# Kernel optimization log

Measured on AMD Instinct MI355X. Metric: run time of the kernel, lower is better.

The kernel has to match this reference:

```python
import jax, jax.numpy as jnp
import numpy as np
from jax.scipy.special import logsumexp

P = 2.0          # geomloss p=2 -> cost = 0.5*|x-y|^2, eps = blur**2
BLUR = 0.05
SCALING = 0.5    # geomloss default annealing factor
K = 16           # fixed-length eps schedule (covers diameter/blur up to ~2^15)


def _softmin(eps, C, h):
    # softmin_i = -eps * logsumexp_j( h_j - C[i,j]/eps )
    return -eps * logsumexp(h[None, :] - C / eps, axis=1)


def _sinkhorn_one(x, y):
    # x, y: (N,) 1D point clouds, uniform weights a=b=1/N
    N = x.shape[0]
    C = 0.5 * (x[:, None] - y[None, :]) ** 2          # (N, N) cost, p=2
    a_log = jnp.full((N,), -jnp.log(jnp.float32(N)))
    b_log = a_log

    # geomloss scaling_parameters: diameter of the joint support (D=1)
    diam = jnp.maximum(x.max(), y.max()) - jnp.minimum(x.min(), y.min())
    eps0 = diam ** 2
    ks = jnp.arange(K)
    # schedule: [d^p, d^p, d^p*s^p, d^p*s^2p, ...] floored at blur^p
    eps_arr = jnp.maximum(BLUR ** 2, eps0 * (SCALING ** 2) ** jnp.maximum(ks - 1, 0))

    # geomloss runs the annealing loop with autograd disabled (implicit diff):
    Cs = jax.lax.stop_gradient(C)
    f = _softmin(eps_arr[0], Cs, b_log)       # potential on x
    g = _softmin(eps_arr[0], Cs.T, a_log)     # potential on y

    def body(carry, eps):
        f, g = carry
        ft = _softmin(eps, Cs, b_log + g / eps)
        gt = _softmin(eps, Cs.T, a_log + f / eps)
        return (0.5 * (f + ft), 0.5 * (g + gt)), None

    (f, g), _ = jax.lax.scan(body, (f, g), eps_arr)
    f = jax.lax.stop_gradient(f)
    g = jax.lax.stop_gradient(g)

    # last extrapolation step at eps = blur^p, with gradients (debias=False)
    eps = BLUR ** 2
    f_fin = _softmin(eps, C, b_log + g / eps)
    g_fin = _softmin(eps, C.T, a_log + f / eps)

    # OT_eps = <a, f> + <b, g>
    return jnp.mean(f_fin) + jnp.mean(g_fin)


def setup_inputs() -> dict:
    key = jax.random.key(0)
    kx, ky = jax.random.split(key)
    B, N = 16, 1536
    x = jax.random.normal(kx, (B, N), dtype=jnp.float32)
    y = jax.random.normal(ky, (B, N), dtype=jnp.float32)
    return {"x": x, "y": y}


def reference(x, y):
    # sum of per-sample Sinkhorn losses (equivalent to the Python loop)
    return jnp.sum(jax.vmap(_sinkhorn_one)(x, y))
```

## Files before the change

### kernel.cpp

```cpp
#include <hip/hip_runtime.h>
#include <math.h>


static constexpr int   BN    = 16;
static constexpr int   NP    = 1536;
static constexpr float BLUR2 = 0.0025f;
static constexpr float L2E   = 1.4426950408889634f;
static constexpr float LN2   = 0.6931471805599453f;
static constexpr float HLOG  = -7.33693691f;

#if defined(__has_builtin)
#if __has_builtin(__builtin_amdgcn_exp2f)
#define EXP2F(x) __builtin_amdgcn_exp2f(x)
#else
#define EXP2F(x) exp2f(x)
#endif
#else
#define EXP2F(x) exp2f(x)
#endif

__global__ __launch_bounds__(256) void sk_setup(const float* __restrict__ x,
                                                const float* __restrict__ y,
                                                float* __restrict__ eps0) {
    const int b = blockIdx.x;
    const int t = threadIdx.x;
    float mn = INFINITY, mx = -INFINITY;
    for (int j = t; j < NP; j += 256) {
        float xv = x[b * NP + j], yv = y[b * NP + j];
        mn = fminf(mn, fminf(xv, yv));
        mx = fmaxf(mx, fmaxf(xv, yv));
    }
    for (int o = 1; o < 64; o <<= 1) {
        mn = fminf(mn, __shfl_xor(mn, o));
        mx = fmaxf(mx, __shfl_xor(mx, o));
    }
    __shared__ float smn[4], smx[4];
    const int w = t >> 6;
    if ((t & 63) == 0) { smn[w] = mn; smx[w] = mx; }
    __syncthreads();
    if (t == 0) {
        mn = fminf(fminf(smn[0], smn[1]), fminf(smn[2], smn[3]));
        mx = fmaxf(fmaxf(smx[0], smx[1]), fmaxf(smx[2], smx[3]));
        float d = mx - mn;
        eps0[b] = d * d;
    }
}

__global__ __launch_bounds__(256) void sk_round(const float* __restrict__ x,
                                                const float* __restrict__ y,
                                                float* __restrict__ ws,
                                                float* __restrict__ out,
                                                int round) {
    __shared__ __align__(16) float2 cu[NP];
    __shared__ float wsum[4];

    const int blk    = blockIdx.x;
    const int batch  = blk / 48;
    const int rb     = blk % 48;
    const int dir    = (rb < 24) ? 0 : 1;
    const int rowblk = rb - dir * 24;

    float* F0 = ws + 16;
    float* F1 = F0 + BN * NP;
    float* G0 = F1 + BN * NP;
    float* G1 = G0 + BN * NP;
    const int ri = (round + 1) & 1;
    const int wi = round & 1;
    float* Fr = ri ? F1 : F0;  float* Fw = wi ? F1 : F0;
    float* Gr = ri ? G1 : G0;  float* Gw = wi ? G1 : G0;

    const float* colc; const float* rowc; const float* hsrc;
    float* obuf; const float* oldb;
    if (dir == 0) {
        colc = y + batch * NP; rowc = x + batch * NP;
        hsrc = Gr + batch * NP; obuf = Fw + batch * NP; oldb = Fr + batch * NP;
    } else {
        colc = x + batch * NP; rowc = y + batch * NP;
        hsrc = Fr + batch * NP; obuf = Gw + batch * NP; oldb = Gr + batch * NP;
    }

    const float e0 = ws[batch];
    float eps;
    if (round == 0)       eps = fmaxf(BLUR2, e0);
    else if (round >= 17) eps = BLUR2;
    else {
        int mk = round - 2; if (mk < 0) mk = 0;
        eps = fmaxf(BLUR2, e0 / (float)(1u << (2 * mk)));
    }
    const float ieps = 1.0f / eps;
    const float c    = 0.5f * ieps;
    const float cL   = c * L2E;

    const int t = threadIdx.x;
    for (int j = t; j < NP; j += 256) {
        float cj = colc[j];
        float hj = (round == 0) ? HLOG : fmaf(hsrc[j], ieps, HLOG);
        float U  = L2E * hj - cL * cj * cj;
        cu[j] = make_float2(cj, U);
    }
    __syncthreads();

    const int lc = t & 3;
    const int lr = t >> 2;
    const int i  = rowblk * 64 + lr;
    const float xi = rowc[i];
    const float S  = 2.0f * cL * xi;
    const float Kc = -cL * xi * xi;

    const float4* p = (const float4*)cu;

    float m0 = -INFINITY, m1 = -INFINITY;
    #pragma unroll 4
    for (int q = lc; q < NP / 2; q += 4) {
        float4 a = p[q];
        m0 = fmaxf(m0, fmaf(S, a.x, a.y));
        m1 = fmaxf(m1, fmaf(S, a.z, a.w));
    }
    float m = fmaxf(m0, m1);
    m = fmaxf(m, __shfl_xor(m, 1));
    m = fmaxf(m, __shfl_xor(m, 2));

    float s0 = 0.0f, s1 = 0.0f;
    #pragma unroll 4
    for (int q = lc; q < NP / 2; q += 4) {
        float4 a = p[q];
        s0 += EXP2F(fmaf(S, a.x, a.y) - m);
        s1 += EXP2F(fmaf(S, a.z, a.w) - m);
    }
    float s = s0 + s1;
    s += __shfl_xor(s, 1);
    s += __shfl_xor(s, 2);

    const float ft = -eps * LN2 * (m + __log2f(s) + Kc);

    if (round < 17) {
        if (lc == 0) {
            float v = (round == 0) ? ft : 0.5f * (oldb[i] + ft);
            obuf[i] = v;
        }
    } else {
        float v = (lc == 0) ? ft : 0.0f;
        for (int o = 1; o < 64; o <<= 1) v += __shfl_xor(v, o);
        const int w = t >> 6;
        if ((t & 63) == 0) wsum[w] = v;
        __syncthreads();
        if (t == 0) {
            float tot = (wsum[0] + wsum[1]) + (wsum[2] + wsum[3]);
            atomicAdd(out, tot * (1.0f / NP));
        }
    }
}

extern "C" void kernel_launch(void* const* d_in, const int* in_sizes, int n_in,
                              void* d_out, int out_size, void* d_ws, size_t ws_size,
                              hipStream_t stream) {
    const float* x = (const float*)d_in[0];
    const float* y = (const float*)d_in[1];
    float* out = (float*)d_out;
    float* ws  = (float*)d_ws;

    hipMemsetAsync(out, 0, sizeof(float), stream);
    hipLaunchKernelGGL(sk_setup, dim3(BN), dim3(256), 0, stream, x, y, ws);
    for (int r = 0; r < 18; ++r) {
        hipLaunchKernelGGL(sk_round, dim3(768), dim3(256), 0, stream,
                           x, y, ws, out, r);
    }
}
```

Before: 400.8 us.

## Register-block eight rows per 32-lane group to reuse LDS column loads

Measured after the change: 370.3 us. 1.08x faster.

```diff
diff --git a/kernel.cpp b/kernel.cpp
--- a/kernel.cpp
+++ b/kernel.cpp
@@ -95,51 +95,80 @@
     for (int j = t; j < NP; j += 256) {
         float cj = colc[j];
         float hj = (round == 0) ? HLOG : fmaf(hsrc[j], ieps, HLOG);
-        float U  = L2E * hj - cL * cj * cj;
+        float U  = fmaf(L2E, hj, -cL * cj * cj);
         cu[j] = make_float2(cj, U);
     }
     __syncthreads();
 
-    const int lc = t & 3;
-    const int lr = t >> 2;
-    const int i  = rowblk * 64 + lr;
-    const float xi = rowc[i];
-    const float S  = 2.0f * cL * xi;
-    const float Kc = -cL * xi * xi;
+    const int l  = t & 31;
+    const int g  = t >> 5;
+    const int i0 = rowblk * 64 + g * 8;
+
+    float S[8], Kc[8];
+    #pragma unroll
+    for (int r = 0; r < 8; ++r) {
+        float xi = rowc[i0 + r];
+        S[r]  = 2.0f * cL * xi;
+        Kc[r] = -cL * xi * xi;
+    }
 
     const float4* p = (const float4*)cu;
 
-    float m0 = -INFINITY, m1 = -INFINITY;
-    #pragma unroll 4
-    for (int q = lc; q < NP / 2; q += 4) {
+    float m[8];
+    #pragma unroll
+    for (int r = 0; r < 8; ++r) m[r] = -INFINITY;
+    #pragma unroll 2
+    for (int q = l; q < NP / 2; q += 32) {
         float4 a = p[q];
-        m0 = fmaxf(m0, fmaf(S, a.x, a.y));
-        m1 = fmaxf(m1, fmaf(S, a.z, a.w));
+        #pragma unroll
+        for (int r = 0; r < 8; ++r) {
+            m[r] = fmaxf(m[r], fmaf(S[r], a.x, a.y));
+            m[r] = fmaxf(m[r], fmaf(S[r], a.z, a.w));
+        }
     }
-    float m = fmaxf(m0, m1);
-    m = fmaxf(m, __shfl_xor(m, 1));
-    m = fmaxf(m, __shfl_xor(m, 2));
+    #pragma unroll
+    for (int r = 0; r < 8; ++r) {
+        m[r] = fmaxf(m[r], __shfl_xor(m[r], 1));
+        m[r] = fmaxf(m[r], __shfl_xor(m[r], 2));
+        m[r] = fmaxf(m[r], __shfl_xor(m[r], 4));
+        m[r] = fmaxf(m[r], __shfl_xor(m[r], 8));
+        m[r] = fmaxf(m[r], __shfl_xor(m[r], 16));
+    }
 
-    float s0 = 0.0f, s1 = 0.0f;
-    #pragma unroll 4
-    for (int q = lc; q < NP / 2; q += 4) {
+    float s[8];
+    #pragma unroll
+    for (int r = 0; r < 8; ++r) s[r] = 0.0f;
+    #pragma unroll 2
+    for (int q = l; q < NP / 2; q += 32) {
         float4 a = p[q];
-        s0 += EXP2F(fmaf(S, a.x, a.y) - m);
-        s1 += EXP2F(fmaf(S, a.z, a.w) - m);
+        #pragma unroll
+        for (int r = 0; r < 8; ++r) {
+            s[r] += EXP2F(fmaf(S[r], a.x, a.y) - m[r]);
+            s[r] += EXP2F(fmaf(S[r], a.z, a.w) - m[r]);
+        }
     }
-    float s = s0 + s1;
-    s += __shfl_xor(s, 1);
-    s += __shfl_xor(s, 2);
+    #pragma unroll
+    for (int r = 0; r < 8; ++r) {
+        s[r] += __shfl_xor(s[r], 1);
+        s[r] += __shfl_xor(s[r], 2);
+        s[r] += __shfl_xor(s[r], 4);
+        s[r] += __shfl_xor(s[r], 8);
+        s[r] += __shfl_xor(s[r], 16);
+    }
 
-    const float ft = -eps * LN2 * (m + __log2f(s) + Kc);
+    float ftv = 0.0f;
+    if (l < 8) {
+        const int r = l;
+        ftv = -eps * LN2 * (m[r] + __log2f(s[r]) + Kc[r]);
+    }
 
     if (round < 17) {
-        if (lc == 0) {
-            float v = (round == 0) ? ft : 0.5f * (oldb[i] + ft);
-            obuf[i] = v;
+        if (l < 8) {
+            const int i = i0 + l;
+            obuf[i] = (round == 0) ? ftv : 0.5f * (oldb[i] + ftv);
         }
     } else {
-        float v = (lc == 0) ? ft : 0.0f;
+        float v = ftv;
         for (int o = 1; o < 64; o <<= 1) v += __shfl_xor(v, o);
         const int w = t >> 6;
         if ((t & 63) == 0) wsum[w] = v;
```
